# Kernel tuning notes

Measured on AMD Instinct MI355X. Metric: run time of the kernel, lower is better.

The kernel has to match this reference:

```python
import jax, jax.numpy as jnp
import numpy as np

K = 3          # kernel_size
STRIDE = 1
PAD = 1
DIL = 1


def setup_inputs() -> dict:
    key = jax.random.key(0)
    k1, k2, k3, k4, k5 = jax.random.split(key, 5)
    x = jax.random.normal(k1, (4, 64, 128, 128), jnp.float32)
    weight = jax.random.normal(k2, (64, 64, K, K), jnp.float32) * 0.05   # [O, C, K, K]
    bias = jax.random.normal(k3, (64,), jnp.float32) * 0.05
    # offset conv params: small nonzero so offsets actually exercise bilinear sampling
    offset_w = jax.random.normal(k4, (2 * K * K, 64, K, K), jnp.float32) * 0.01
    offset_b = jax.random.normal(k5, (2 * K * K,), jnp.float32) * 0.1
    return {"x": x, "weight": weight, "bias": bias,
            "offset_w": offset_w, "offset_b": offset_b}


def _conv2d(x, w, b):
    y = jax.lax.conv_general_dilated(
        x, w, window_strides=(STRIDE, STRIDE),
        padding=((PAD, PAD), (PAD, PAD)), rhs_dilation=(DIL, DIL),
        dimension_numbers=("NCHW", "OIHW", "NCHW"))
    return y + b[None, :, None, None]


def _bilinear_sample(img, ys, xs):
    # img: [C, H, W]; ys, xs: [KK, Ho, Wo] float sampling coords
    H, W = img.shape[1], img.shape[2]
    y0 = jnp.floor(ys)
    x0 = jnp.floor(xs)
    y1 = y0 + 1.0
    x1 = x0 + 1.0
    wy1 = ys - y0
    wx1 = xs - x0
    wy0 = 1.0 - wy1
    wx0 = 1.0 - wx1

    def gather(yy, xx):
        valid = (yy >= 0) & (yy <= H - 1) & (xx >= 0) & (xx <= W - 1)
        yi = jnp.clip(yy, 0, H - 1).astype(jnp.int32)
        xi = jnp.clip(xx, 0, W - 1).astype(jnp.int32)
        v = img[:, yi, xi]                     # [C, KK, Ho, Wo]
        return v * valid.astype(img.dtype)

    return (gather(y0, x0) * (wy0 * wx0) + gather(y0, x1) * (wy0 * wx1)
            + gather(y1, x0) * (wy1 * wx0) + gather(y1, x1) * (wy1 * wx1))


def reference(x, weight, bias, offset_w, offset_b):
    B, C, H, W = x.shape
    KK = K * K
    # offsets: [B, 2*K*K, Ho, Wo], per-location (dy, dx) for each kernel tap
    offset = _conv2d(x, offset_w, offset_b)
    Ho, Wo = offset.shape[2], offset.shape[3]
    off = offset.reshape(B, KK, 2, Ho, Wo)
    dy, dx = off[:, :, 0], off[:, :, 1]        # [B, KK, Ho, Wo]

    ki, kj = jnp.meshgrid(jnp.arange(K), jnp.arange(K), indexing="ij")
    ki = ki.reshape(KK).astype(x.dtype)
    kj = kj.reshape(KK).astype(x.dtype)
    oy = (jnp.arange(Ho) * STRIDE - PAD).astype(x.dtype)
    ox = (jnp.arange(Wo) * STRIDE - PAD).astype(x.dtype)
    base_y = oy[None, :, None] + (ki * DIL)[:, None, None]   # [KK, Ho, 1]
    base_x = ox[None, None, :] + (kj * DIL)[:, None, None]   # [KK, 1, Wo]
    ys = base_y[None] + dy                                   # [B, KK, Ho, Wo]
    xs = base_x[None] + dx

    # sampled: [B, C, KK, Ho, Wo]
    sampled = jax.vmap(_bilinear_sample)(x, ys, xs)
    w = weight.reshape(weight.shape[0], C, KK)
    out = jnp.einsum("bckhw,ock->bohw", sampled, w) + bias[None, :, None, None]
    return out
```

## Files before the change

### kernel.cpp

```cpp
#include <hip/hip_runtime.h>
#include <hip/hip_bf16.h>

#define B_ 4
#define C_ 64
#define H_ 128
#define W_ 128
#define HW_ (H_ * W_)
#define OCH_ 18

typedef __attribute__((ext_vector_type(2)))  _Float16 half2v;
typedef __attribute__((ext_vector_type(8)))  _Float16 half8;
typedef __attribute__((ext_vector_type(16))) float    f32x16;

#define W2B_ELEMS (9 * 2 * 4 * 64 * 8)
#define W2A_ELEMS (36 * 64 * 8)

#define PSTRIDE_B (6 * 128 * 16 + 16)
#define WIN_BYTES (8 * PSTRIDE_B)
#define OFFL_OFS  WIN_BYTES
#define OFFW_B    (OCH_ * 32 * 4)
#define SMEM_BYTES (WIN_BYTES + 8 * OFFW_B)

__device__ __forceinline__ unsigned short f2h(float f) {
  _Float16 h = (_Float16)f;
  return *reinterpret_cast<unsigned short*>(&h);
}
__device__ __forceinline__ half2v pkrtz(float a, float b) {
  auto p = __builtin_amdgcn_cvt_pkrtz(a, b);
  return *reinterpret_cast<half2v*>(&p);
}
__device__ __forceinline__ int swz256(int x) { return (x & 7) * 32 + (x >> 3); }
__device__ __forceinline__ int SWU(int row, int col) {
  return (((row << 7) + (col & ~3) + ((col & 3) ^ ((col >> 3) & 3))) << 4);
}

__global__ __launch_bounds__(256) void pack_w_only(
    const float* __restrict__ wmain, const float* __restrict__ offw,
    unsigned short* __restrict__ ws_u) {
  int idx = blockIdx.x * 256 + threadIdx.x;
  if (idx < W2B_ELEMS) {
    int i = idx & 7, lane = (idx >> 3) & 63, s = (idx >> 9) & 3;
    int mq = (idx >> 11) & 1, t = idx >> 12;
    int o = mq * 32 + (lane & 31);
    int c = 16 * s + (lane >> 5) * 8 + i;
    ws_u[idx] = f2h(wmain[(o * 64 + c) * 9 + t]);
  } else if (idx < W2B_ELEMS + W2A_ELEMS) {
    int j = idx - W2B_ELEMS;
    int i = j & 7, lane = (j >> 3) & 63, s = j >> 9;
    int kg = 16 * s + (lane >> 5) * 8 + i;
    int t = kg >> 6, c = kg & 63, oc = lane & 31;
    ws_u[idx] = (oc < OCH_) ? f2h(offw[(oc * 64 + c) * 9 + t]) : (unsigned short)0;
  }
}

template<int T>
__device__ __forceinline__ void tap_fast(
    const float* __restrict__ offl, int pxl, int ho, int ho0, int px,
    int lane, int laneh, const char* __restrict__ smem,
    const unsigned short* __restrict__ w2b,
    f32x16& acc0, f32x16& acc1, unsigned& fm) {
  constexpr int KI = T / 3, KJ = T - 3 * (T / 3);
  const float dy = offl[(2 * T) * 32 + pxl];
  const float dx = offl[(2 * T + 1) * 32 + pxl];
  const float ys = (float)(ho - 1 + KI) + dy;
  const float xs = (float)(px - 1 + KJ) + dx;
  const float y0f = floorf(ys), x0f = floorf(xs);
  const int y0 = (int)y0f, x0 = (int)x0f;
  const int y1 = y0 + 1, x1 = x0 + 1;
  const float wy1 = ys - y0f, wx1 = xs - x0f;
  const float wy0 = 1.f - wy1, wx0 = 1.f - wx1;
  const bool vy0 = (unsigned)y0 < (unsigned)H_, vy1 = (unsigned)y1 < (unsigned)H_;
  const bool vx0 = (unsigned)x0 < (unsigned)W_, vx1 = (unsigned)x1 < (unsigned)W_;
  const float g00 = (vy0 && vx0) ? wy0 * wx0 : 0.f;
  const float g01 = (vy0 && vx1) ? wy0 * wx1 : 0.f;
  const float g10 = (vy1 && vx0) ? wy1 * wx0 : 0.f;
  const float g11 = (vy1 && vx1) ? wy1 * wx1 : 0.f;
  const int yc0 = min(max(y0, 0), H_ - 1), yc1 = min(max(y1, 0), H_ - 1);
  const int xc0 = min(max(x0, 0), W_ - 1), xc1 = min(max(x1, 0), W_ - 1);
  const int rr0 = yc0 - ho0 + 2, rr1 = yc1 - ho0 + 2;
  const bool wr0 = (unsigned)rr0 < 6u, wr1 = (unsigned)rr1 < 6u;
  const float gg00 = wr0 ? g00 : 0.f, gg01 = wr0 ? g01 : 0.f;
  const float gg10 = wr1 ? g10 : 0.f, gg11 = wr1 ? g11 : 0.f;
  if (__any((!wr0 & (vy0 & (vx0 | vx1))) | (!wr1 & (vy1 & (vx0 | vx1)))))
    fm |= (1u << T);
  const int cr0 = min(max(rr0, 0), 5), cr1 = min(max(rr1, 0), 5);
  const int u00 = SWU(cr0, xc0), u01 = SWU(cr0, xc1);
  const int u10 = SWU(cr1, xc0), u11 = SWU(cr1, xc1);
  half2v G00; G00.x = G00.y = (_Float16)gg00;
  half2v G01; G01.x = G01.y = (_Float16)gg01;
  half2v G10; G10.x = G10.y = (_Float16)gg10;
  half2v G11; G11.x = G11.y = (_Float16)gg11;
  const unsigned short* wt2 = w2b + T * 4096;

  __builtin_amdgcn_s_setprio(1);
  #pragma unroll
  for (int ss = 0; ss < 4; ++ss) {
    const char* pb = smem + (2 * ss + laneh) * PSTRIDE_B;
    const half8 c00 = *(const half8*)(pb + u00);
    const half8 c01 = *(const half8*)(pb + u01);
    const half8 c10 = *(const half8*)(pb + u10);
    const half8 c11 = *(const half8*)(pb + u11);
    const half2v* p00 = (const half2v*)&c00;
    const half2v* p01 = (const half2v*)&c01;
    const half2v* p10 = (const half2v*)&c10;
    const half2v* p11 = (const half2v*)&c11;
    union { half8 v; half2v h[4]; } bf;
    #pragma unroll
    for (int d = 0; d < 4; ++d)
      bf.h[d] = p00[d] * G00 + p01[d] * G01 + p10[d] * G10 + p11[d] * G11;
    const half8 a0 = *(const half8*)&wt2[(ss * 64 + lane) * 8];
    const half8 a1 = *(const half8*)&wt2[((4 + ss) * 64 + lane) * 8];
    acc0 = __builtin_amdgcn_mfma_f32_32x32x16_f16(a0, bf.v, acc0, 0, 0, 0);
    acc1 = __builtin_amdgcn_mfma_f32_32x32x16_f16(a1, bf.v, acc1, 0, 0, 0);
  }
  __builtin_amdgcn_s_setprio(0);
}

__global__ __launch_bounds__(512, 2) void deform_fused12(
    const float* __restrict__ x, const float* __restrict__ bias,
    const float* __restrict__ ob, const unsigned short* __restrict__ w2b,
    const unsigned short* __restrict__ w2a, float* __restrict__ out) {
  const int blk = swz256(blockIdx.x);
  const int ho0 = (blk & 63) * 2;
  const int b   = blk >> 6;
  const int tid = threadIdx.x;
  const int lane = tid & 63;
  const int wave = tid >> 6;
  const int r_off = wave >> 2;
  const int pair  = wave & 3;
  const int ho = ho0 + r_off;
  const int pxl = lane & 31;
  const int px = pair * 32 + pxl;
  const int laneh = lane >> 5;

  __shared__ __align__(16) char smem[SMEM_BYTES];

  const float* xb = x + (size_t)b * C_ * HW_;
  #pragma unroll
  for (int it = 0; it < 3; ++it) {
    const int u = tid + it * 512;
    const int row  = u >> 8;
    const int p    = (u >> 5) & 7;
    const int col4 = u & 31;
    const int srow = min(H_ - 1, max(0, ho0 - 2 + row));
    const float* bp = xb + (size_t)(p * 8) * HW_ + srow * W_ + col4 * 4;
    float4 f[8];
    #pragma unroll
    for (int i = 0; i < 8; ++i) f[i] = *(const float4*)(bp + (size_t)i * HW_);
    char* outb = smem + p * PSTRIDE_B;
    #pragma unroll
    for (int j = 0; j < 4; ++j) {
      union { half8 v; half2v h[4]; } o;
      #pragma unroll
      for (int k = 0; k < 4; ++k)
        o.h[k] = pkrtz(reinterpret_cast<const float*>(&f[2 * k])[j],
                       reinterpret_cast<const float*>(&f[2 * k + 1])[j]);
      *(half8*)(outb + SWU(row, col4 * 4 + j)) = o.v;
    }
  }
  __syncthreads();

  f32x16 pacc_a, pacc_b;
  #pragma unroll
  for (int r = 0; r < 16; ++r) { pacc_a[r] = 0.f; pacc_b[r] = 0.f; }

  #pragma unroll 1
  for (int sq = 0; sq < 18; ++sq) {
    #pragma unroll
    for (int h = 0; h < 2; ++h) {
      const int s = 2 * sq + h;
      const int t = s >> 2;
      const int ki = (t >= 6) ? 2 : ((t >= 3) ? 1 : 0);
      const int kj = t - 3 * ki;
      const int row = ho - 1 + ki;
      const int col = px - 1 + kj;
      half8 bfr = {0, 0, 0, 0, 0, 0, 0, 0};
      if (((unsigned)row < (unsigned)H_) && ((unsigned)col < (unsigned)W_))
        bfr = *(const half8*)(smem + ((s & 3) * 2 + laneh) * PSTRIDE_B
                              + SWU(ki + 1 + r_off, col));
      const half8 afr = *(const half8*)&w2a[((size_t)s * 64 + lane) * 8];
      if (h)
        pacc_b = __builtin_amdgcn_mfma_f32_32x32x16_f16(afr, bfr, pacc_b, 0, 0, 0);
      else
        pacc_a = __builtin_amdgcn_mfma_f32_32x32x16_f16(afr, bfr, pacc_a, 0, 0, 0);
    }
  }

  float* offl = (float*)(smem + OFFL_OFS + wave * OFFW_B);
  #pragma unroll
  for (int reg = 0; reg < 16; ++reg) {
    const int oc = (reg & 3) + 8 * (reg >> 2) + 4 * laneh;
    if (oc < OCH_) offl[oc * 32 + pxl] = pacc_a[reg] + pacc_b[reg] + ob[oc];
  }

  f32x16 acc0, acc1;
  #pragma unroll
  for (int r = 0; r < 16; ++r) { acc0[r] = 0.f; acc1[r] = 0.f; }
  unsigned fm = 0;

  tap_fast<0>(offl, pxl, ho, ho0, px, lane, laneh, smem, w2b, acc0, acc1, fm);
  tap_fast<1>(offl, pxl, ho, ho0, px, lane, laneh, smem, w2b, acc0, acc1, fm);
  tap_fast<2>(offl, pxl, ho, ho0, px, lane, laneh, smem, w2b, acc0, acc1, fm);
  tap_fast<3>(offl, pxl, ho, ho0, px, lane, laneh, smem, w2b, acc0, acc1, fm);
  tap_fast<4>(offl, pxl, ho, ho0, px, lane, laneh, smem, w2b, acc0, acc1, fm);
  tap_fast<5>(offl, pxl, ho, ho0, px, lane, laneh, smem, w2b, acc0, acc1, fm);
  tap_fast<6>(offl, pxl, ho, ho0, px, lane, laneh, smem, w2b, acc0, acc1, fm);
  tap_fast<7>(offl, pxl, ho, ho0, px, lane, laneh, smem, w2b, acc0, acc1, fm);
  tap_fast<8>(offl, pxl, ho, ho0, px, lane, laneh, smem, w2b, acc0, acc1, fm);

  if (__builtin_expect(fm != 0, 0)) {
    #pragma unroll 1
    for (int t = 0; t < 9; ++t) {
      if (!((fm >> t) & 1)) continue;
      const int ki = (t >= 6) ? 2 : ((t >= 3) ? 1 : 0);
      const int kj = t - 3 * ki;
      const float dy = offl[(2 * t) * 32 + pxl];
      const float dx = offl[(2 * t + 1) * 32 + pxl];
      const float ys = (float)(ho - 1 + ki) + dy;
      const float xs = (float)(px - 1 + kj) + dx;
      const float y0f = floorf(ys), x0f = floorf(xs);
      const int y0 = (int)y0f, x0 = (int)x0f;
      const int y1 = y0 + 1, x1 = x0 + 1;
      const float wy1 = ys - y0f, wx1 = xs - x0f;
      const float wy0 = 1.f - wy1, wx0 = 1.f - wx1;
      const bool vy0 = (unsigned)y0 < (unsigned)H_, vy1 = (unsigned)y1 < (unsigned)H_;
      const bool vx0 = (unsigned)x0 < (unsigned)W_, vx1 = (unsigned)x1 < (unsigned)W_;
      float g00 = (vy0 && vx0) ? wy0 * wx0 : 0.f;
      float g01 = (vy0 && vx1) ? wy0 * wx1 : 0.f;
      float g10 = (vy1 && vx0) ? wy1 * wx0 : 0.f;
      float g11 = (vy1 && vx1) ? wy1 * wx1 : 0.f;
      const int yc0 = min(max(y0, 0), H_ - 1), yc1 = min(max(y1, 0), H_ - 1);
      const int xc0 = min(max(x0, 0), W_ - 1), xc1 = min(max(x1, 0), W_ - 1);
      const bool wr0 = (unsigned)(yc0 - ho0 + 2) < 6u;
      const bool wr1 = (unsigned)(yc1 - ho0 + 2) < 6u;
      g00 = wr0 ? 0.f : g00; g01 = wr0 ? 0.f : g01;
      g10 = wr1 ? 0.f : g10; g11 = wr1 ? 0.f : g11;
      const unsigned short* wt2 = w2b + t * 4096;
      #pragma unroll 1
      for (int ss = 0; ss < 4; ++ss) {
        union { half8 v; _Float16 e[8]; } bf;
        #pragma unroll
        for (int i = 0; i < 8; ++i) {
          const float* img = xb + (size_t)((2 * ss + laneh) * 8 + i) * HW_;
          float v = g00 * img[yc0 * W_ + xc0] + g01 * img[yc0 * W_ + xc1]
                  + g10 * img[yc1 * W_ + xc0] + g11 * img[yc1 * W_ + xc1];
          bf.e[i] = (_Float16)v;
        }
        const half8 a0 = *(const half8*)&wt2[(ss * 64 + lane) * 8];
        const half8 a1 = *(const half8*)&wt2[((4 + ss) * 64 + lane) * 8];
        acc0 = __builtin_amdgcn_mfma_f32_32x32x16_f16(a0, bf.v, acc0, 0, 0, 0);
        acc1 = __builtin_amdgcn_mfma_f32_32x32x16_f16(a1, bf.v, acc1, 0, 0, 0);
      }
    }
  }

  #pragma unroll
  for (int reg = 0; reg < 16; ++reg) {
    const int row = (reg & 3) + 8 * (reg >> 2) + 4 * laneh;
    out[((b * 64 + row)      * H_ + ho) * W_ + px] = acc0[reg] + bias[row];
    out[((b * 64 + 32 + row) * H_ + ho) * W_ + px] = acc1[reg] + bias[32 + row];
  }
}

extern "C" void kernel_launch(void* const* d_in, const int* in_sizes, int n_in,
                              void* d_out, int out_size, void* d_ws, size_t ws_size,
                              hipStream_t stream) {
  const float* x    = (const float*)d_in[0];
  const float* wt   = (const float*)d_in[1];
  const float* bias = (const float*)d_in[2];
  const float* ow   = (const float*)d_in[3];
  const float* ob   = (const float*)d_in[4];
  float* out = (float*)d_out;

  unsigned short* ws_u = (unsigned short*)d_ws;
  unsigned short* w2b  = ws_u;
  unsigned short* w2a  = ws_u + W2B_ELEMS;

  const int pack_blocks = (W2B_ELEMS + W2A_ELEMS + 255) / 256;
  pack_w_only<<<pack_blocks, 256, 0, stream>>>(wt, ow, ws_u);

  deform_fused12<<<B_ * (H_ / 2), 512, 0, stream>>>(x, bias, ob, w2b, w2a, out);
}
```

Measured before the change: 37.02 us.

## Split channel reduction across two wave halves with 1024-thread blocks

The kernel doubles the block to 1024 threads and splits the channel reduction (K dimension) of both the offset conv and the deformable sampling/MFMA work between two wave groups. Partial offset sums are exchanged through shared memory, and the final accumulators are reduced through shared memory before the store. The goal is more waves per CU, to hide LDS and gather latency, and shorter per-wave serial chains. In exchange it adds extra syncthreads, a shared-memory reduction, duplicated bilinear coordinate math in both halves, and it drops the LDS row padding, which may cause bank conflicts.

```diff
diff --git a/kernel.cpp b/kernel.cpp
--- a/kernel.cpp
+++ b/kernel.cpp
@@ -15,11 +15,10 @@
 #define W2B_ELEMS (9 * 2 * 4 * 64 * 8)
 #define W2A_ELEMS (36 * 64 * 8)
 
-#define PSTRIDE_B (6 * 128 * 16 + 16)
+#define PSTRIDE_B (6 * 128 * 16)
 #define WIN_BYTES (8 * PSTRIDE_B)
-#define OFFL_OFS  WIN_BYTES
-#define OFFW_B    (OCH_ * 32 * 4)
-#define SMEM_BYTES (WIN_BYTES + 8 * OFFW_B)
+#define OFFP_OFS  WIN_BYTES
+#define SMEM_BYTES (WIN_BYTES + 2 * 8 * OCH_ * 32 * 4)
 
 __device__ __forceinline__ unsigned short f2h(float f) {
   _Float16 h = (_Float16)f;
@@ -53,15 +52,13 @@
   }
 }
 
-template<int T>
+template<int T, int SSH>
 __device__ __forceinline__ void tap_fast(
-    const float* __restrict__ offl, int pxl, int ho, int ho0, int px,
+    float dy, float dx, int ho, int ho0, int px,
     int lane, int laneh, const char* __restrict__ smem,
     const unsigned short* __restrict__ w2b,
     f32x16& acc0, f32x16& acc1, unsigned& fm) {
   constexpr int KI = T / 3, KJ = T - 3 * (T / 3);
-  const float dy = offl[(2 * T) * 32 + pxl];
-  const float dx = offl[(2 * T + 1) * 32 + pxl];
   const float ys = (float)(ho - 1 + KI) + dy;
   const float xs = (float)(px - 1 + KJ) + dx;
   const float y0f = floorf(ys), x0f = floorf(xs);
@@ -94,7 +91,8 @@
 
   __builtin_amdgcn_s_setprio(1);
   #pragma unroll
-  for (int ss = 0; ss < 4; ++ss) {
+  for (int j = 0; j < 2; ++j) {
+    const int ss = 2 * SSH + j;
     const char* pb = smem + (2 * ss + laneh) * PSTRIDE_B;
     const half8 c00 = *(const half8*)(pb + u00);
     const half8 c01 = *(const half8*)(pb + u01);
@@ -116,7 +114,51 @@
   __builtin_amdgcn_s_setprio(0);
 }
 
-__global__ __launch_bounds__(512, 2) void deform_fused12(
+template<int T, int SSH>
+__device__ __forceinline__ void tap_fix(
+    float dy, float dx, int ho, int ho0, int px, int lane, int laneh,
+    const float* __restrict__ xb, const unsigned short* __restrict__ w2b,
+    f32x16& acc0, f32x16& acc1) {
+  constexpr int KI = T / 3, KJ = T - 3 * (T / 3);
+  const float ys = (float)(ho - 1 + KI) + dy;
+  const float xs = (float)(px - 1 + KJ) + dx;
+  const float y0f = floorf(ys), x0f = floorf(xs);
+  const int y0 = (int)y0f, x0 = (int)x0f;
+  const int y1 = y0 + 1, x1 = x0 + 1;
+  const float wy1 = ys - y0f, wx1 = xs - x0f;
+  const float wy0 = 1.f - wy1, wx0 = 1.f - wx1;
+  const bool vy0 = (unsigned)y0 < (unsigned)H_, vy1 = (unsigned)y1 < (unsigned)H_;
+  const bool vx0 = (unsigned)x0 < (unsigned)W_, vx1 = (unsigned)x1 < (unsigned)W_;
+  float g00 = (vy0 && vx0) ? wy0 * wx0 : 0.f;
+  float g01 = (vy0 && vx1) ? wy0 * wx1 : 0.f;
+  float g10 = (vy1 && vx0) ? wy1 * wx0 : 0.f;
+  float g11 = (vy1 && vx1) ? wy1 * wx1 : 0.f;
+  const int yc0 = min(max(y0, 0), H_ - 1), yc1 = min(max(y1, 0), H_ - 1);
+  const int xc0 = min(max(x0, 0), W_ - 1), xc1 = min(max(x1, 0), W_ - 1);
+  const bool wr0 = (unsigned)(yc0 - ho0 + 2) < 6u;
+  const bool wr1 = (unsigned)(yc1 - ho0 + 2) < 6u;
+  g00 = wr0 ? 0.f : g00; g01 = wr0 ? 0.f : g01;
+  g10 = wr1 ? 0.f : g10; g11 = wr1 ? 0.f : g11;
+  const unsigned short* wt2 = w2b + T * 4096;
+  #pragma unroll
+  for (int j = 0; j < 2; ++j) {
+    const int ss = 2 * SSH + j;
+    union { half8 v; _Float16 e[8]; } bf;
+    #pragma unroll
+    for (int i = 0; i < 8; ++i) {
+      const float* img = xb + (size_t)((2 * ss + laneh) * 8 + i) * HW_;
+      float v = g00 * img[yc0 * W_ + xc0] + g01 * img[yc0 * W_ + xc1]
+              + g10 * img[yc1 * W_ + xc0] + g11 * img[yc1 * W_ + xc1];
+      bf.e[i] = (_Float16)v;
+    }
+    const half8 a0 = *(const half8*)&wt2[(ss * 64 + lane) * 8];
+    const half8 a1 = *(const half8*)&wt2[((4 + ss) * 64 + lane) * 8];
+    acc0 = __builtin_amdgcn_mfma_f32_32x32x16_f16(a0, bf.v, acc0, 0, 0, 0);
+    acc1 = __builtin_amdgcn_mfma_f32_32x32x16_f16(a1, bf.v, acc1, 0, 0, 0);
+  }
+}
+
+__global__ __launch_bounds__(1024, 4) void deform_fused14(
     const float* __restrict__ x, const float* __restrict__ bias,
     const float* __restrict__ ob, const unsigned short* __restrict__ w2b,
     const unsigned short* __restrict__ w2a, float* __restrict__ out) {
@@ -126,8 +168,10 @@
   const int tid = threadIdx.x;
   const int lane = tid & 63;
   const int wave = tid >> 6;
-  const int r_off = wave >> 2;
+  const int ssh   = wave >> 3;
+  const int r_off = (wave >> 2) & 1;
   const int pair  = wave & 3;
+  const int w7    = r_off * 4 + pair;
   const int ho = ho0 + r_off;
   const int pxl = lane & 31;
   const int px = pair * 32 + pxl;
@@ -137,25 +181,27 @@
 
   const float* xb = x + (size_t)b * C_ * HW_;
   #pragma unroll
-  for (int it = 0; it < 3; ++it) {
-    const int u = tid + it * 512;
-    const int row  = u >> 8;
-    const int p    = (u >> 5) & 7;
-    const int col4 = u & 31;
-    const int srow = min(H_ - 1, max(0, ho0 - 2 + row));
-    const float* bp = xb + (size_t)(p * 8) * HW_ + srow * W_ + col4 * 4;
-    float4 f[8];
-    #pragma unroll
-    for (int i = 0; i < 8; ++i) f[i] = *(const float4*)(bp + (size_t)i * HW_);
-    char* outb = smem + p * PSTRIDE_B;
-    #pragma unroll
-    for (int j = 0; j < 4; ++j) {
-      union { half8 v; half2v h[4]; } o;
+  for (int it = 0; it < 2; ++it) {
+    const int u = tid + it * 1024;
+    if (u < 1536) {
+      const int row  = u >> 8;
+      const int p    = (u >> 5) & 7;
+      const int col4 = u & 31;
+      const int srow = min(H_ - 1, max(0, ho0 - 2 + row));
+      const float* bp = xb + (size_t)(p * 8) * HW_ + srow * W_ + col4 * 4;
+      float4 f[8];
       #pragma unroll
-      for (int k = 0; k < 4; ++k)
-        o.h[k] = pkrtz(reinterpret_cast<const float*>(&f[2 * k])[j],
-                       reinterpret_cast<const float*>(&f[2 * k + 1])[j]);
-      *(half8*)(outb + SWU(row, col4 * 4 + j)) = o.v;
+      for (int i = 0; i < 8; ++i) f[i] = *(const float4*)(bp + (size_t)i * HW_);
+      char* outb = smem + p * PSTRIDE_B;
+      #pragma unroll
+      for (int j = 0; j < 4; ++j) {
+        union { half8 v; half2v h[4]; } o;
+        #pragma unroll
+        for (int k = 0; k < 4; ++k)
+          o.h[k] = pkrtz(reinterpret_cast<const float*>(&f[2 * k])[j],
+                         reinterpret_cast<const float*>(&f[2 * k + 1])[j]);
+        *(half8*)(outb + SWU(row, col4 * 4 + j)) = o.v;
+      }
     }
   }
   __syncthreads();
@@ -165,100 +211,110 @@
   for (int r = 0; r < 16; ++r) { pacc_a[r] = 0.f; pacc_b[r] = 0.f; }
 
   #pragma unroll 1
-  for (int sq = 0; sq < 18; ++sq) {
-    #pragma unroll
-    for (int h = 0; h < 2; ++h) {
-      const int s = 2 * sq + h;
-      const int t = s >> 2;
-      const int ki = (t >= 6) ? 2 : ((t >= 3) ? 1 : 0);
-      const int kj = t - 3 * ki;
-      const int row = ho - 1 + ki;
-      const int col = px - 1 + kj;
-      half8 bfr = {0, 0, 0, 0, 0, 0, 0, 0};
-      if (((unsigned)row < (unsigned)H_) && ((unsigned)col < (unsigned)W_))
-        bfr = *(const half8*)(smem + ((s & 3) * 2 + laneh) * PSTRIDE_B
-                              + SWU(ki + 1 + r_off, col));
-      const half8 afr = *(const half8*)&w2a[((size_t)s * 64 + lane) * 8];
-      if (h)
-        pacc_b = __builtin_amdgcn_mfma_f32_32x32x16_f16(afr, bfr, pacc_b, 0, 0, 0);
-      else
-        pacc_a = __builtin_amdgcn_mfma_f32_32x32x16_f16(afr, bfr, pacc_a, 0, 0, 0);
-    }
-  }
-
-  float* offl = (float*)(smem + OFFL_OFS + wave * OFFW_B);
+  for (int q = 0; q < 18; ++q) {
+    const int s = 2 * q + ssh;
+    const int t = s >> 2;
+    const int ki = (t >= 6) ? 2 : ((t >= 3) ? 1 : 0);
+    const int kj = t - 3 * ki;
+    const int row = ho - 1 + ki;
+    const int col = px - 1 + kj;
+    half8 bfr = {0, 0, 0, 0, 0, 0, 0, 0};
+    if (((unsigned)row < (unsigned)H_) && ((unsigned)col < (unsigned)W_))
+      bfr = *(const half8*)(smem + ((s & 3) * 2 + laneh) * PSTRIDE_B
+                            + SWU(ki + 1 + r_off, col));
+    const half8 afr = *(const half8*)&w2a[((size_t)s * 64 + lane) * 8];
+    if (q & 1)
+      pacc_b = __builtin_amdgcn_mfma_f32_32x32x16_f16(afr, bfr, pacc_b, 0, 0, 0);
+    else
+      pacc_a = __builtin_amdgcn_mfma_f32_32x32x16_f16(afr, bfr, pacc_a, 0, 0, 0);
+  }
+
+  float* offp = (float*)(smem + OFFP_OFS);
   #pragma unroll
   for (int reg = 0; reg < 16; ++reg) {
     const int oc = (reg & 3) + 8 * (reg >> 2) + 4 * laneh;
-    if (oc < OCH_) offl[oc * 32 + pxl] = pacc_a[reg] + pacc_b[reg] + ob[oc];
-  }
+    if (oc < OCH_)
+      offp[((ssh * 8 + w7) * OCH_ + oc) * 32 + pxl] = pacc_a[reg] + pacc_b[reg];
+  }
+  __syncthreads();
+
+  const float* oA = offp + (w7 * OCH_) * 32 + pxl;
+  const float* oB = offp + ((8 + w7) * OCH_) * 32 + pxl;
+  float dv[18];
+  #pragma unroll
+  for (int k = 0; k < 18; ++k) dv[k] = oA[k * 32] + oB[k * 32] + ob[k];
 
   f32x16 acc0, acc1;
   #pragma unroll
   for (int r = 0; r < 16; ++r) { acc0[r] = 0.f; acc1[r] = 0.f; }
   unsigned fm = 0;
 
-  tap_fast<0>(offl, pxl, ho, ho0, px, lane, laneh, smem, w2b, acc0, acc1, fm);
-  tap_fast<1>(offl, pxl, ho, ho0, px, lane, laneh, smem, w2b, acc0, acc1, fm);
-  tap_fast<2>(offl, pxl, ho, ho0, px, lane, laneh, smem, w2b, acc0, acc1, fm);
-  tap_fast<3>(offl, pxl, ho, ho0, px, lane, laneh, smem, w2b, acc0, acc1, fm);
-  tap_fast<4>(offl, pxl, ho, ho0, px, lane, laneh, smem, w2b, acc0, acc1, fm);
-  tap_fast<5>(offl, pxl, ho, ho0, px, lane, laneh, smem, w2b, acc0, acc1, fm);
-  tap_fast<6>(offl, pxl, ho, ho0, px, lane, laneh, smem, w2b, acc0, acc1, fm);
-  tap_fast<7>(offl, pxl, ho, ho0, px, lane, laneh, smem, w2b, acc0, acc1, fm);
-  tap_fast<8>(offl, pxl, ho, ho0, px, lane, laneh, smem, w2b, acc0, acc1, fm);
-
-  if (__builtin_expect(fm != 0, 0)) {
-    #pragma unroll 1
-    for (int t = 0; t < 9; ++t) {
-      if (!((fm >> t) & 1)) continue;
-      const int ki = (t >= 6) ? 2 : ((t >= 3) ? 1 : 0);
-      const int kj = t - 3 * ki;
-      const float dy = offl[(2 * t) * 32 + pxl];
-      const float dx = offl[(2 * t + 1) * 32 + pxl];
-      const float ys = (float)(ho - 1 + ki) + dy;
-      const float xs = (float)(px - 1 + kj) + dx;
-      const float y0f = floorf(ys), x0f = floorf(xs);
-      const int y0 = (int)y0f, x0 = (int)x0f;
-      const int y1 = y0 + 1, x1 = x0 + 1;
-      const float wy1 = ys - y0f, wx1 = xs - x0f;
-      const float wy0 = 1.f - wy1, wx0 = 1.f - wx1;
-      const bool vy0 = (unsigned)y0 < (unsigned)H_, vy1 = (unsigned)y1 < (unsigned)H_;
-      const bool vx0 = (unsigned)x0 < (unsigned)W_, vx1 = (unsigned)x1 < (unsigned)W_;
-      float g00 = (vy0 && vx0) ? wy0 * wx0 : 0.f;
-      float g01 = (vy0 && vx1) ? wy0 * wx1 : 0.f;
-      float g10 = (vy1 && vx0) ? wy1 * wx0 : 0.f;
-      float g11 = (vy1 && vx1) ? wy1 * wx1 : 0.f;
-      const int yc0 = min(max(y0, 0), H_ - 1), yc1 = min(max(y1, 0), H_ - 1);
-      const int xc0 = min(max(x0, 0), W_ - 1), xc1 = min(max(x1, 0), W_ - 1);
-      const bool wr0 = (unsigned)(yc0 - ho0 + 2) < 6u;
-      const bool wr1 = (unsigned)(yc1 - ho0 + 2) < 6u;
-      g00 = wr0 ? 0.f : g00; g01 = wr0 ? 0.f : g01;
-      g10 = wr1 ? 0.f : g10; g11 = wr1 ? 0.f : g11;
-      const unsigned short* wt2 = w2b + t * 4096;
-      #pragma unroll 1
-      for (int ss = 0; ss < 4; ++ss) {
-        union { half8 v; _Float16 e[8]; } bf;
-        #pragma unroll
-        for (int i = 0; i < 8; ++i) {
-          const float* img = xb + (size_t)((2 * ss + laneh) * 8 + i) * HW_;
-          float v = g00 * img[yc0 * W_ + xc0] + g01 * img[yc0 * W_ + xc1]
-                  + g10 * img[yc1 * W_ + xc0] + g11 * img[yc1 * W_ + xc1];
-          bf.e[i] = (_Float16)v;
-        }
-        const half8 a0 = *(const half8*)&wt2[(ss * 64 + lane) * 8];
-        const half8 a1 = *(const half8*)&wt2[((4 + ss) * 64 + lane) * 8];
-        acc0 = __builtin_amdgcn_mfma_f32_32x32x16_f16(a0, bf.v, acc0, 0, 0, 0);
-        acc1 = __builtin_amdgcn_mfma_f32_32x32x16_f16(a1, bf.v, acc1, 0, 0, 0);
-      }
-    }
-  }
-
-  #pragma unroll
-  for (int reg = 0; reg < 16; ++reg) {
-    const int row = (reg & 3) + 8 * (reg >> 2) + 4 * laneh;
-    out[((b * 64 + row)      * H_ + ho) * W_ + px] = acc0[reg] + bias[row];
-    out[((b * 64 + 32 + row) * H_ + ho) * W_ + px] = acc1[reg] + bias[32 + row];
+  if (ssh == 0) {
+    tap_fast<0, 0>(dv[0],  dv[1],  ho, ho0, px, lane, laneh, smem, w2b, acc0, acc1, fm);
+    tap_fast<1, 0>(dv[2],  dv[3],  ho, ho0, px, lane, laneh, smem, w2b, acc0, acc1, fm);
+    tap_fast<2, 0>(dv[4],  dv[5],  ho, ho0, px, lane, laneh, smem, w2b, acc0, acc1, fm);
+    tap_fast<3, 0>(dv[6],  dv[7],  ho, ho0, px, lane, laneh, smem, w2b, acc0, acc1, fm);
+    tap_fast<4, 0>(dv[8],  dv[9],  ho, ho0, px, lane, laneh, smem, w2b, acc0, acc1, fm);
+    tap_fast<5, 0>(dv[10], dv[11], ho, ho0, px, lane, laneh, smem, w2b, acc0, acc1, fm);
+    tap_fast<6, 0>(dv[12], dv[13], ho, ho0, px, lane, laneh, smem, w2b, acc0, acc1, fm);
+    tap_fast<7, 0>(dv[14], dv[15], ho, ho0, px, lane, laneh, smem, w2b, acc0, acc1, fm);
+    tap_fast<8, 0>(dv[16], dv[17], ho, ho0, px, lane, laneh, smem, w2b, acc0, acc1, fm);
+    if (__builtin_expect(fm != 0, 0)) {
+      if (fm & 1)   tap_fix<0, 0>(dv[0],  dv[1],  ho, ho0, px, lane, laneh, xb, w2b, acc0, acc1);
+      if (fm & 2)   tap_fix<1, 0>(dv[2],  dv[3],  ho, ho0, px, lane, laneh, xb, w2b, acc0, acc1);
+      if (fm & 4)   tap_fix<2, 0>(dv[4],  dv[5],  ho, ho0, px, lane, laneh, xb, w2b, acc0, acc1);
+      if (fm & 8)   tap_fix<3, 0>(dv[6],  dv[7],  ho, ho0, px, lane, laneh, xb, w2b, acc0, acc1);
+      if (fm & 16)  tap_fix<4, 0>(dv[8],  dv[9],  ho, ho0, px, lane, laneh, xb, w2b, acc0, acc1);
+      if (fm & 32)  tap_fix<5, 0>(dv[10], dv[11], ho, ho0, px, lane, laneh, xb, w2b, acc0, acc1);
+      if (fm & 64)  tap_fix<6, 0>(dv[12], dv[13], ho, ho0, px, lane, laneh, xb, w2b, acc0, acc1);
+      if (fm & 128) tap_fix<7, 0>(dv[14], dv[15], ho, ho0, px, lane, laneh, xb, w2b, acc0, acc1);
+      if (fm & 256) tap_fix<8, 0>(dv[16], dv[17], ho, ho0, px, lane, laneh, xb, w2b, acc0, acc1);
+    }
+  } else {
+    tap_fast<0, 1>(dv[0],  dv[1],  ho, ho0, px, lane, laneh, smem, w2b, acc0, acc1, fm);
+    tap_fast<1, 1>(dv[2],  dv[3],  ho, ho0, px, lane, laneh, smem, w2b, acc0, acc1, fm);
+    tap_fast<2, 1>(dv[4],  dv[5],  ho, ho0, px, lane, laneh, smem, w2b, acc0, acc1, fm);
+    tap_fast<3, 1>(dv[6],  dv[7],  ho, ho0, px, lane, laneh, smem, w2b, acc0, acc1, fm);
+    tap_fast<4, 1>(dv[8],  dv[9],  ho, ho0, px, lane, laneh, smem, w2b, acc0, acc1, fm);
+    tap_fast<5, 1>(dv[10], dv[11], ho, ho0, px, lane, laneh, smem, w2b, acc0, acc1, fm);
+    tap_fast<6, 1>(dv[12], dv[13], ho, ho0, px, lane, laneh, smem, w2b, acc0, acc1, fm);
+    tap_fast<7, 1>(dv[14], dv[15], ho, ho0, px, lane, laneh, smem, w2b, acc0, acc1, fm);
+    tap_fast<8, 1>(dv[16], dv[17], ho, ho0, px, lane, laneh, smem, w2b, acc0, acc1, fm);
+    if (__builtin_expect(fm != 0, 0)) {
+      if (fm & 1)   tap_fix<0, 1>(dv[0],  dv[1],  ho, ho0, px, lane, laneh, xb, w2b, acc0, acc1);
+      if (fm & 2)   tap_fix<1, 1>(dv[2],  dv[3],  ho, ho0, px, lane, laneh, xb, w2b, acc0, acc1);
+      if (fm & 4)   tap_fix<2, 1>(dv[4],  dv[5],  ho, ho0, px, lane, laneh, xb, w2b, acc0, acc1);
+      if (fm & 8)   tap_fix<3, 1>(dv[6],  dv[7],  ho, ho0, px, lane, laneh, xb, w2b, acc0, acc1);
+      if (fm & 16)  tap_fix<4, 1>(dv[8],  dv[9],  ho, ho0, px, lane, laneh, xb, w2b, acc0, acc1);
+      if (fm & 32)  tap_fix<5, 1>(dv[10], dv[11], ho, ho0, px, lane, laneh, xb, w2b, acc0, acc1);
+      if (fm & 64)  tap_fix<6, 1>(dv[12], dv[13], ho, ho0, px, lane, laneh, xb, w2b, acc0, acc1);
+      if (fm & 128) tap_fix<7, 1>(dv[14], dv[15], ho, ho0, px, lane, laneh, xb, w2b, acc0, acc1);
+      if (fm & 256) tap_fix<8, 1>(dv[16], dv[17], ho, ho0, px, lane, laneh, xb, w2b, acc0, acc1);
+    }
+  }
+
+  __syncthreads();
+  float* red = (float*)smem;
+  if (ssh) {
+    #pragma unroll
+    for (int i = 0; i < 16; ++i) {
+      red[(i * 8 + w7) * 64 + lane]          = acc0[i];
+      red[((16 + i) * 8 + w7) * 64 + lane]   = acc1[i];
+    }
+  }
+  __syncthreads();
+  if (!ssh) {
+    #pragma unroll
+    for (int i = 0; i < 16; ++i) {
+      acc0[i] += red[(i * 8 + w7) * 64 + lane];
+      acc1[i] += red[((16 + i) * 8 + w7) * 64 + lane];
+    }
+    #pragma unroll
+    for (int reg = 0; reg < 16; ++reg) {
+      const int row = (reg & 3) + 8 * (reg >> 2) + 4 * laneh;
+      out[((b * 64 + row)      * H_ + ho) * W_ + px] = acc0[reg] + bias[row];
+      out[((b * 64 + 32 + row) * H_ + ho) * W_ + px] = acc1[reg] + bias[32 + row];
+    }
   }
 }
 
@@ -279,5 +335,5 @@
   const int pack_blocks = (W2B_ELEMS + W2A_ELEMS + 255) / 256;
   pack_w_only<<<pack_blocks, 256, 0, stream>>>(wt, ow, ws_u);
 
-  deform_fused12<<<B_ * (H_ / 2), 512, 0, stream>>>(x, bias, ob, w2b, w2a, out);
-}
+  deform_fused14<<<B_ * (H_ / 2), 1024, 0, stream>>>(x, bias, ob, w2b, w2a, out);
+}
```

Result: slower. 43.15 us (+16.5%).
